# Performance work log

Measured on AMD Instinct MI355X. Metric: run time of the kernel, lower is better.

Reference implementation:

```python
import jax, jax.numpy as jnp
import numpy as np


def _pair_loss(s, r):
    # s: [N, 4] sampled lidar, r: [M, 4] raw lidar; use xyz only
    a = s[:, :3]
    b = r[:, :3]
    # pairwise Euclidean distances, [N, M] (torch.cdist p=2)
    sq = (jnp.sum(a * a, axis=1)[:, None]
          + jnp.sum(b * b, axis=1)[None, :]
          - 2.0 * (a @ b.T))
    dist = jnp.sqrt(jnp.maximum(sq, 0.0))
    # dist[argmin(dim=0), j] == min over rows; dist[i, argmin(dim=1)] == min over cols
    min_over_sampled = jnp.min(dist, axis=0)  # [M] nearest sampled point per raw point
    min_over_raw = jnp.min(dist, axis=1)      # [N] nearest raw point per sampled point
    LB = jnp.mean(min_over_sampled)
    LF = jnp.mean(min_over_raw)
    LM = jnp.max(min_over_raw)
    return 5.0 * LB + 1.0 * LF + LM


def setup_inputs() -> dict:
    key = jax.random.key(0)
    k1, k2 = jax.random.split(key)
    B, N, M = 2, 4096, 16384
    sampled = jax.random.normal(k1, (B, N, 4), dtype=jnp.float32)
    raw = jax.random.normal(k2, (B, M, 4), dtype=jnp.float32)
    return {"sampled": sampled, "raw": raw}


def reference(sampled, raw):
    # list of pairs == batch dim; loss averaged over pairs
    losses = jax.vmap(_pair_loss)(sampled, raw)  # [B]
    return jnp.mean(losses)
```

## Files before the change

### kernel.cpp

```cpp
#include <hip/hip_runtime.h>
#include <math.h>

constexpr int BB = 2, NN = 4096, MM = 16384;
constexpr int JS = 32;
constexpr int IG = 16;
constexpr int SC = 512;
constexpr int ST = SC / 32;
constexpr unsigned INFBITS = 0x7F800000u;
constexpr ushort ONEB = 0x3F80;

typedef __attribute__((ext_vector_type(8)))  short  short8;
typedef __attribute__((ext_vector_type(8)))  ushort ushort8;
typedef __attribute__((ext_vector_type(16))) float  f32x16;

__device__ __forceinline__ ushort f2bf(float f) {
    unsigned u = __float_as_uint(f);
    u += 0x7FFF + ((u >> 16) & 1);
    return (ushort)(u >> 16);
}
__device__ __forceinline__ void split2(float v, ushort& h, ushort& l) {
    h = f2bf(v);
    l = f2bf(v - __uint_as_float(((unsigned)h) << 16));
}
__device__ __forceinline__ float vmin16(const f32x16& c) {
    float a0 = fminf(fminf(c[0], c[1]),  fminf(c[2], c[3]));
    float a1 = fminf(fminf(c[4], c[5]),  fminf(c[6], c[7]));
    float a2 = fminf(fminf(c[8], c[9]),  fminf(c[10], c[11]));
    float a3 = fminf(fminf(c[12], c[13]), fminf(c[14], c[15]));
    return fminf(fminf(a0, a1), fminf(a2, a3));
}

__global__ __launch_bounds__(256, 4) void pair_kernel(
    const float* __restrict__ sampled,
    const float* __restrict__ raw,
    float* __restrict__ rowpart,
    float* __restrict__ colpart,
    unsigned* __restrict__ counter)
{
    __shared__ ushort ldsB[ST * 512];
    __shared__ float  ldsCol[4][SC];

    const int js = blockIdx.x, ig = blockIdx.y, b = blockIdx.z;
    const int tid = threadIdx.x, w = tid >> 6, lane = tid & 63;
    const int j0 = js * SC, i0 = ig * 256;

    if (js == 0 && ig == 0 && b == 0 && tid == 0) *counter = 0u;

    const float4* rp4 = (const float4*)raw + (size_t)b * MM + j0;
    for (int t = tid; t < SC; t += 256) {
        float4 v = rp4[t];
        float n = fmaf(v.z, v.z, fmaf(v.y, v.y, v.x * v.x));
        ushort hx,lx,hy,ly,hz,lz,hn,ln;
        split2(v.x, hx, lx); split2(v.y, hy, ly);
        split2(v.z, hz, lz); split2(n, hn, ln);
        ushort* dst = ldsB + (t >> 5) * 512 + (t & 31) * 8;
        *(ushort8*)(dst)       = ushort8{hx,hy,hz,lx,ly,lz,hx,hy};
        *(ushort8*)(dst + 256) = ushort8{hz,ONEB,ONEB,hn,ln,0,0,0};
    }

    short8 afr[2];
    const float4* sp4 = (const float4*)sampled + (size_t)b * NN + i0 + w * 64 + (lane & 31);
    const int half = lane >> 5;
#pragma unroll
    for (int f = 0; f < 2; ++f) {
        float4 v = sp4[f * 32];
        float n = fmaf(v.z, v.z, fmaf(v.y, v.y, v.x * v.x));
        ushort hx,lx,hy,ly,hz,lz,hn,ln;
        split2(-2.f * v.x, hx, lx); split2(-2.f * v.y, hy, ly);
        split2(-2.f * v.z, hz, lz); split2(n, hn, ln);
        ushort8 w0 = ushort8{hx,hy,hz,hx,hy,hz,lx,ly};
        ushort8 w1 = ushort8{lz,hn,ln,ONEB,ONEB,0,0,0};
        ushort8 sel = half ? w1 : w0;
        afr[f] = *(short8*)&sel;
    }
    __syncthreads();

    const float INF = __uint_as_float(INFBITS);
    float racc0[16], racc1[16];
#pragma unroll
    for (int r = 0; r < 16; ++r) { racc0[r] = INF; racc1[r] = INF; }

    const f32x16 zero = {0.f,0.f,0.f,0.f,0.f,0.f,0.f,0.f,
                         0.f,0.f,0.f,0.f,0.f,0.f,0.f,0.f};

#pragma unroll 1
    for (int jt = 0; jt < ST; ++jt) {
        short8 bf = *(const short8*)(ldsB + jt * 512 + lane * 8);
        f32x16 c0 = __builtin_amdgcn_mfma_f32_32x32x16_bf16(afr[0], bf, zero, 0, 0, 0);
        f32x16 c1 = __builtin_amdgcn_mfma_f32_32x32x16_bf16(afr[1], bf, zero, 0, 0, 0);
#pragma unroll
        for (int r = 0; r < 16; ++r) {
            racc0[r] = fminf(racc0[r], c0[r]);
            racc1[r] = fminf(racc1[r], c1[r]);
        }
        float m = fminf(vmin16(c0), vmin16(c1));
        m = fminf(m, __shfl_xor(m, 32, 64));
        if (lane < 32) ldsCol[w][jt * 32 + lane] = m;
    }

#pragma unroll
    for (int mask = 1; mask < 32; mask <<= 1) {
#pragma unroll
        for (int r = 0; r < 16; ++r) {
            racc0[r] = fminf(racc0[r], __shfl_xor(racc0[r], mask, 64));
            racc1[r] = fminf(racc1[r], __shfl_xor(racc1[r], mask, 64));
        }
    }
    if ((lane & 31) == 0) {
        float* rp = rowpart + ((size_t)js * BB + b) * NN + i0 + w * 64;
#pragma unroll
        for (int r = 0; r < 16; ++r) {
            const int row = (r & 3) + 8 * (r >> 2) + 4 * half;
            rp[row]      = fmaxf(racc0[r], 0.f);
            rp[32 + row] = fmaxf(racc1[r], 0.f);
        }
    }

    __syncthreads();
    float* cp = colpart + ((size_t)ig * BB + b) * MM + j0;
    for (int t = tid; t < SC; t += 256) {
        float v = fminf(fminf(ldsCol[0][t], ldsCol[1][t]),
                        fminf(ldsCol[2][t], ldsCol[3][t]));
        cp[t] = fmaxf(v, 0.f);
    }
}

__global__ __launch_bounds__(256) void reduce_kernel(
    const float* __restrict__ rowpart,
    const float* __restrict__ colpart,
    float* __restrict__ part,
    unsigned* __restrict__ counter,
    float* __restrict__ out)
{
    const int k = blockIdx.x, b = k >> 6, s = k & 63;
    const int tid = threadIdx.x;
    const float INF = __uint_as_float(INFBITS);

    const int col = s * 256 + tid;
    float v = INF;
#pragma unroll 4
    for (int ig = 0; ig < IG; ++ig)
        v = fminf(v, colpart[((size_t)ig * BB + b) * MM + col]);
    float sB = sqrtf(v);

    const int row = s * 64 + (tid & 63);
    const int jq  = tid >> 6;
    float wv2 = INF;
#pragma unroll
    for (int q = 0; q < JS / 4; ++q)
        wv2 = fminf(wv2, rowpart[((size_t)(jq * (JS / 4) + q) * BB + b) * NN + row]);
    __shared__ float rred[4][64];
    rred[jq][tid & 63] = wv2;
    __syncthreads();
    float sF = 0.f, mF = 0.f;
    if (tid < 64) {
        float rmn = fminf(fminf(rred[0][tid], rred[1][tid]),
                          fminf(rred[2][tid], rred[3][tid]));
        float d = sqrtf(rmn);
        sF = d; mF = d;
    }

    for (int m = 1; m < 64; m <<= 1) {
        sB += __shfl_xor(sB, m, 64);
        sF += __shfl_xor(sF, m, 64);
        mF = fmaxf(mF, __shfl_xor(mF, m, 64));
    }
    __shared__ float red[3][4];
    const int lane = tid & 63, wvi = tid >> 6;
    if (lane == 0) { red[0][wvi] = sB; red[1][wvi] = sF; red[2][wvi] = mF; }
    __syncthreads();

    __shared__ bool isLast;
    if (tid == 0) {
        part[k * 3 + 0] = red[0][0] + red[0][1] + red[0][2] + red[0][3];
        part[k * 3 + 1] = red[1][0] + red[1][1] + red[1][2] + red[1][3];
        part[k * 3 + 2] = fmaxf(fmaxf(red[2][0], red[2][1]),
                                fmaxf(red[2][2], red[2][3]));
        __threadfence();
        isLast = (atomicAdd(counter, 1u) == 127u);
    }
    __syncthreads();
    if (!isLast) return;

    __threadfence();
    volatile const float* vp = part;
    float fB = 0.f, fF = 0.f, fM = 0.f;
    if (tid < 128) {
        fB = vp[tid * 3 + 0]; fF = vp[tid * 3 + 1]; fM = vp[tid * 3 + 2];
    }
    for (int m = 1; m < 64; m <<= 1) {
        fB += __shfl_xor(fB, m, 64);
        fF += __shfl_xor(fF, m, 64);
        fM = fmaxf(fM, __shfl_xor(fM, m, 64));
    }
    __shared__ float fin[2][3];
    if (tid < 128 && (tid & 63) == 0) {
        fin[tid >> 6][0] = fB; fin[tid >> 6][1] = fF; fin[tid >> 6][2] = fM;
    }
    __syncthreads();
    if (tid == 0) {
        float l0 = 5.f * fin[0][0] / (float)MM + fin[0][1] / (float)NN + fin[0][2];
        float l1 = 5.f * fin[1][0] / (float)MM + fin[1][1] / (float)NN + fin[1][2];
        *out = 0.5f * (l0 + l1);
    }
}

extern "C" void kernel_launch(void* const* d_in, const int* in_sizes, int n_in,
                              void* d_out, int out_size, void* d_ws, size_t ws_size,
                              hipStream_t stream) {
    const float* sampled = (const float*)d_in[0];
    const float* raw     = (const float*)d_in[1];
    float* rowpart = (float*)d_ws;
    float* colpart = rowpart + (size_t)JS * BB * NN;
    float* part    = colpart + (size_t)IG * BB * MM;
    unsigned* counter = (unsigned*)(part + 3 * 128);
    float* out     = (float*)d_out;

    pair_kernel<<<dim3(JS, IG, BB), 256, 0, stream>>>(sampled, raw, rowpart, colpart, counter);
    reduce_kernel<<<128, 256, 0, stream>>>(rowpart, colpart, part, counter, out);
}
```

Baseline: 38.35 us.

## Prepack raw points in separate kernel and halve rows per pair block

Measured after the change: 45.07 us. 1.18x slower.

```diff
diff --git a/kernel.cpp b/kernel.cpp
--- a/kernel.cpp
+++ b/kernel.cpp
@@ -3,7 +3,7 @@
 
 constexpr int BB = 2, NN = 4096, MM = 16384;
 constexpr int JS = 32;
-constexpr int IG = 16;
+constexpr int IG2 = 32;
 constexpr int SC = 512;
 constexpr int ST = SC / 32;
 constexpr unsigned INFBITS = 0x7F800000u;
@@ -23,47 +23,46 @@
     l = f2bf(v - __uint_as_float(((unsigned)h) << 16));
 }
 __device__ __forceinline__ float vmin16(const f32x16& c) {
-    float a0 = fminf(fminf(c[0], c[1]),  fminf(c[2], c[3]));
-    float a1 = fminf(fminf(c[4], c[5]),  fminf(c[6], c[7]));
-    float a2 = fminf(fminf(c[8], c[9]),  fminf(c[10], c[11]));
+    float a0 = fminf(fminf(c[0], c[1]),   fminf(c[2], c[3]));
+    float a1 = fminf(fminf(c[4], c[5]),   fminf(c[6], c[7]));
+    float a2 = fminf(fminf(c[8], c[9]),   fminf(c[10], c[11]));
     float a3 = fminf(fminf(c[12], c[13]), fminf(c[14], c[15]));
     return fminf(fminf(a0, a1), fminf(a2, a3));
 }
 
+__global__ __launch_bounds__(256) void packB_kernel(
+    const float* __restrict__ raw, ushort* __restrict__ Bpack)
+{
+    const int g = blockIdx.x * 256 + threadIdx.x;
+    float4 v = ((const float4*)raw)[g];
+    float n = fmaf(v.z, v.z, fmaf(v.y, v.y, v.x * v.x));
+    ushort hx,lx,hy,ly,hz,lz,hn,ln;
+    split2(v.x, hx, lx); split2(v.y, hy, ly);
+    split2(v.z, hz, lz); split2(n, hn, ln);
+    ushort* dst = Bpack + ((size_t)(g >> 5) << 9) + (g & 31) * 8;
+    *(ushort8*)(dst)       = ushort8{hx,hy,hz,lx,ly,lz,hx,hy};
+    *(ushort8*)(dst + 256) = ushort8{hz,ONEB,ONEB,hn,ln,0,0,0};
+}
+
 __global__ __launch_bounds__(256, 4) void pair_kernel(
     const float* __restrict__ sampled,
-    const float* __restrict__ raw,
+    const ushort* __restrict__ Bpack,
     float* __restrict__ rowpart,
     float* __restrict__ colpart,
     unsigned* __restrict__ counter)
 {
-    __shared__ ushort ldsB[ST * 512];
-    __shared__ float  ldsCol[4][SC];
+    __shared__ float ldsCol[4][SC];
 
     const int js = blockIdx.x, ig = blockIdx.y, b = blockIdx.z;
     const int tid = threadIdx.x, w = tid >> 6, lane = tid & 63;
-    const int j0 = js * SC, i0 = ig * 256;
+    const int half = lane >> 5;
+    const int j0 = js * SC, i0 = ig * 128;
 
     if (js == 0 && ig == 0 && b == 0 && tid == 0) *counter = 0u;
 
-    const float4* rp4 = (const float4*)raw + (size_t)b * MM + j0;
-    for (int t = tid; t < SC; t += 256) {
-        float4 v = rp4[t];
-        float n = fmaf(v.z, v.z, fmaf(v.y, v.y, v.x * v.x));
-        ushort hx,lx,hy,ly,hz,lz,hn,ln;
-        split2(v.x, hx, lx); split2(v.y, hy, ly);
-        split2(v.z, hz, lz); split2(n, hn, ln);
-        ushort* dst = ldsB + (t >> 5) * 512 + (t & 31) * 8;
-        *(ushort8*)(dst)       = ushort8{hx,hy,hz,lx,ly,lz,hx,hy};
-        *(ushort8*)(dst + 256) = ushort8{hz,ONEB,ONEB,hn,ln,0,0,0};
-    }
-
-    short8 afr[2];
-    const float4* sp4 = (const float4*)sampled + (size_t)b * NN + i0 + w * 64 + (lane & 31);
-    const int half = lane >> 5;
-#pragma unroll
-    for (int f = 0; f < 2; ++f) {
-        float4 v = sp4[f * 32];
+    short8 afr;
+    {
+        float4 v = ((const float4*)sampled)[(size_t)b * NN + i0 + w * 32 + (lane & 31)];
         float n = fmaf(v.z, v.z, fmaf(v.y, v.y, v.x * v.x));
         ushort hx,lx,hy,ly,hz,lz,hn,ln;
         split2(-2.f * v.x, hx, lx); split2(-2.f * v.y, hy, ly);
@@ -71,48 +70,40 @@
         ushort8 w0 = ushort8{hx,hy,hz,hx,hy,hz,lx,ly};
         ushort8 w1 = ushort8{lz,hn,ln,ONEB,ONEB,0,0,0};
         ushort8 sel = half ? w1 : w0;
-        afr[f] = *(short8*)&sel;
-    }
-    __syncthreads();
+        afr = *(short8*)&sel;
+    }
 
     const float INF = __uint_as_float(INFBITS);
-    float racc0[16], racc1[16];
-#pragma unroll
-    for (int r = 0; r < 16; ++r) { racc0[r] = INF; racc1[r] = INF; }
+    float racc[16];
+#pragma unroll
+    for (int r = 0; r < 16; ++r) racc[r] = INF;
 
     const f32x16 zero = {0.f,0.f,0.f,0.f,0.f,0.f,0.f,0.f,
                          0.f,0.f,0.f,0.f,0.f,0.f,0.f,0.f};
+    const ushort* Bb = Bpack + (((size_t)(b * (MM / 32) + js * ST)) << 9) + lane * 8;
 
 #pragma unroll 1
     for (int jt = 0; jt < ST; ++jt) {
-        short8 bf = *(const short8*)(ldsB + jt * 512 + lane * 8);
-        f32x16 c0 = __builtin_amdgcn_mfma_f32_32x32x16_bf16(afr[0], bf, zero, 0, 0, 0);
-        f32x16 c1 = __builtin_amdgcn_mfma_f32_32x32x16_bf16(afr[1], bf, zero, 0, 0, 0);
-#pragma unroll
-        for (int r = 0; r < 16; ++r) {
-            racc0[r] = fminf(racc0[r], c0[r]);
-            racc1[r] = fminf(racc1[r], c1[r]);
-        }
-        float m = fminf(vmin16(c0), vmin16(c1));
+        short8 bf = *(const short8*)(Bb + ((size_t)jt << 9));
+        f32x16 c = __builtin_amdgcn_mfma_f32_32x32x16_bf16(afr, bf, zero, 0, 0, 0);
+#pragma unroll
+        for (int r = 0; r < 16; ++r) racc[r] = fminf(racc[r], c[r]);
+        float m = vmin16(c);
         m = fminf(m, __shfl_xor(m, 32, 64));
         if (lane < 32) ldsCol[w][jt * 32 + lane] = m;
     }
 
 #pragma unroll
-    for (int mask = 1; mask < 32; mask <<= 1) {
-#pragma unroll
-        for (int r = 0; r < 16; ++r) {
-            racc0[r] = fminf(racc0[r], __shfl_xor(racc0[r], mask, 64));
-            racc1[r] = fminf(racc1[r], __shfl_xor(racc1[r], mask, 64));
-        }
-    }
+    for (int mask = 1; mask < 32; mask <<= 1)
+#pragma unroll
+        for (int r = 0; r < 16; ++r)
+            racc[r] = fminf(racc[r], __shfl_xor(racc[r], mask, 64));
     if ((lane & 31) == 0) {
-        float* rp = rowpart + ((size_t)js * BB + b) * NN + i0 + w * 64;
+        float* rp = rowpart + ((size_t)js * BB + b) * NN + i0 + w * 32;
 #pragma unroll
         for (int r = 0; r < 16; ++r) {
             const int row = (r & 3) + 8 * (r >> 2) + 4 * half;
-            rp[row]      = fmaxf(racc0[r], 0.f);
-            rp[32 + row] = fmaxf(racc1[r], 0.f);
+            rp[row] = fmaxf(racc[r], 0.f);
         }
     }
 
@@ -139,7 +130,7 @@
     const int col = s * 256 + tid;
     float v = INF;
 #pragma unroll 4
-    for (int ig = 0; ig < IG; ++ig)
+    for (int ig = 0; ig < IG2; ++ig)
         v = fminf(v, colpart[((size_t)ig * BB + b) * MM + col]);
     float sB = sqrtf(v);
 
@@ -210,12 +201,14 @@
                               hipStream_t stream) {
     const float* sampled = (const float*)d_in[0];
     const float* raw     = (const float*)d_in[1];
-    float* rowpart = (float*)d_ws;
+    ushort* Bpack  = (ushort*)d_ws;
+    float* rowpart = (float*)(Bpack + (size_t)BB * MM * 16);
     float* colpart = rowpart + (size_t)JS * BB * NN;
-    float* part    = colpart + (size_t)IG * BB * MM;
+    float* part    = colpart + (size_t)IG2 * BB * MM;
     unsigned* counter = (unsigned*)(part + 3 * 128);
     float* out     = (float*)d_out;
 
-    pair_kernel<<<dim3(JS, IG, BB), 256, 0, stream>>>(sampled, raw, rowpart, colpart, counter);
+    packB_kernel<<<(BB * MM) / 256, 256, 0, stream>>>(raw, Bpack);
+    pair_kernel<<<dim3(JS, IG2, BB), 256, 0, stream>>>(sampled, Bpack, rowpart, colpart, counter);
     reduce_kernel<<<128, 256, 0, stream>>>(rowpart, colpart, part, counter, out);
 }
```
